# Optimization experiments

Hardware: AMD Instinct MI355X
Metric: run time of the kernel (lower is better)

Reference implementation:

```python
import jax, jax.numpy as jnp
import numpy as np

B, S, D, H = 1, 2048, 768, 12
E, K, I = 8, 2, 1024          # routed experts, top-k, expert inter dim
IS = 2 * I                    # shared-expert inter dim (n_shared_experts * moe_inter_dim)
EPS = 1e-5
ROUTE_SCALE = 1.0


def rmsnorm(x, w, eps=EPS):
    xf = x.astype(jnp.float32)
    return (xf * jax.lax.rsqrt(jnp.mean(xf * xf, axis=-1, keepdims=True) + eps)).astype(x.dtype) * w


def setup_inputs() -> dict:
    key = jax.random.key(0)
    ks = jax.random.split(key, 8)
    sc = 0.02
    return {
        "x": jax.random.normal(ks[0], (B, S, D), jnp.float32),
        "norm1_w": jnp.ones((D,), jnp.float32),
        "norm3_w": jnp.ones((D,), jnp.float32),
        "gate_w": jax.random.normal(ks[1], (E, D), jnp.float32) * sc,
        "w1": jax.random.normal(ks[2], (E, I, D), jnp.float32) * sc,
        "b1": jnp.zeros((E, I), jnp.float32),
        "w2": jax.random.normal(ks[3], (E, D, I), jnp.float32) * sc,
        "b2": jnp.zeros((E, D), jnp.float32),
        "w3": jax.random.normal(ks[4], (E, I, D), jnp.float32) * sc,
        "b3": jnp.zeros((E, I), jnp.float32),
        "fc1_w": jax.random.normal(ks[5], (IS, D), jnp.float32) * sc,
        "fc1_b": jnp.zeros((IS,), jnp.float32),
        "fc2_w": jax.random.normal(ks[6], (D, IS), jnp.float32) * sc,
        "fc2_b": jnp.zeros((D,), jnp.float32),
    }


def _forward(x, norm1_w, norm3_w, gate_w, w1, b1, w2, b2, w3, b3,
             fc1_w, fc1_b, fc2_w, fc2_b):
    b, s, d = x.shape
    hd = d // H

    # ---- self-attention (no qkv/out projections in the original module) ----
    xn = rmsnorm(x, norm1_w)
    qkv = xn.reshape(b, s, H, hd).transpose(0, 2, 1, 3)      # [b,h,s,hd]
    scores = jnp.einsum("bhqd,bhkd->bhqk", qkv, qkv) / np.sqrt(hd)
    attn = jax.nn.softmax(scores, axis=-1)
    ao = jnp.einsum("bhqk,bhkd->bhqd", attn, qkv)
    attn_out = ao.transpose(0, 2, 1, 3).reshape(b, s, d)
    out = x + attn_out

    # ---- MoE on norm3(out) ----
    xf = rmsnorm(out, norm3_w).reshape(-1, d)                # [N, D]
    n = xf.shape[0]

    # Gate: softmax scoring, n_groups=1 (no group masking), no bias (dim != 7168)
    logits = xf @ gate_w.T                                    # [N, E]
    sc = jax.nn.softmax(logits.astype(jnp.float32), axis=-1)  # max-subtract folded in
    _, idx = jax.lax.top_k(sc, K)                             # [N, K]
    weights = jnp.take_along_axis(sc, idx, axis=-1)
    weights = jnp.clip(weights, 1e-7) * ROUTE_SCALE
    weights = weights.astype(xf.dtype)

    # combine matrix: per-token dense expert weights (zeros for unselected)
    cmb = jnp.zeros((n, E), xf.dtype).at[jnp.arange(n)[:, None], idx].add(weights)

    # SwiGLU experts, batched over E (zero combine weight == not dispatched)
    a = jnp.einsum("nd,eid->nei", xf, w1) + b1                # [N,E,I]
    g = jnp.einsum("nd,eid->nei", xf, w3) + b3
    h = jax.nn.silu(a) * g
    eo = jnp.einsum("nei,edi->ned", h, w2) + b2               # [N,E,D]
    y = jnp.einsum("ned,ne->nd", eo, cmb)

    # shared experts (SiLU MLP)
    z = jax.nn.silu(xf @ fc1_w.T + fc1_b) @ fc2_w.T + fc2_b

    moe_out = (y + z).reshape(b, s, d)
    return out + moe_out


def reference(x, norm1_w, norm3_w, gate_w, w1, b1, w2, b2, w3, b3,
              fc1_w, fc1_b, fc2_w, fc2_b):
    return _forward(x, norm1_w, norm3_w, gate_w, w1, b1, w2, b2, w3, b3,
                    fc1_w, fc1_b, fc2_w, fc2_b)
```

## Files before the change

### kernel.cpp

```cpp
#include <hip/hip_runtime.h>
#include <math.h>

#define SEQ    2048
#define DMODEL 768
#define NHEAD  12
#define NEXP   8
#define IDIM   1024
#define ISH    2048
#define KVS    4
#define NE2    10

typedef unsigned short u16;
typedef short s16x8 __attribute__((ext_vector_type(8)));
typedef u16   u16x8 __attribute__((ext_vector_type(8)));
typedef float f32x4 __attribute__((ext_vector_type(4)));

#define MFMA_BF16(a, b, c) __builtin_amdgcn_mfma_f32_16x16x32_bf16((a), (b), (c), 0, 0, 0)

__device__ __forceinline__ void glds16(const void* g, void* l) {
  __builtin_amdgcn_global_load_lds(
      (const __attribute__((address_space(1))) unsigned int*)g,
      (__attribute__((address_space(3))) unsigned int*)l, 16, 0, 0);
}

__device__ __forceinline__ u16 f2b(float f) {
  unsigned int u = __float_as_uint(f);
  unsigned int r = u + 0x7fffu + ((u >> 16) & 1u);
  return (u16)(r >> 16);
}
__device__ __forceinline__ float b2f(u16 v) {
  return __uint_as_float(((unsigned int)v) << 16);
}

__global__ __launch_bounds__(256) void cvt_all_kernel(
    const float* __restrict__ w1, const float* __restrict__ w3, const float* __restrict__ w2,
    const float* __restrict__ fc1, const float* __restrict__ fc2,
    u16* __restrict__ w1b, u16* __restrict__ w3b, u16* __restrict__ w2b,
    u16* __restrict__ fc1b, u16* __restrict__ fc2b, int* __restrict__ counts) {
  if (blockIdx.x == 0 && threadIdx.x < 16) counts[threadIdx.x] = 0;
  long i = (long)blockIdx.x * 256 + threadIdx.x;
  const long NW8 = (long)NEXP * IDIM * DMODEL / 8;
  const long NF8 = (long)ISH * DMODEL / 8;
  const float* s; u16* d; long o;
  if      (i < NW8)             { s = w1;  d = w1b;  o = i; }
  else if (i < 2 * NW8)         { s = w3;  d = w3b;  o = i - NW8; }
  else if (i < 3 * NW8)         { s = w2;  d = w2b;  o = i - 2 * NW8; }
  else if (i < 3 * NW8 + NF8)   { s = fc1; d = fc1b; o = i - 3 * NW8; }
  else if (i < 3 * NW8 + 2*NF8) { s = fc2; d = fc2b; o = i - 3 * NW8 - NF8; }
  else return;
  float4 a = ((const float4*)s)[2 * o], b = ((const float4*)s)[2 * o + 1];
  u16x8 v;
  v[0] = f2b(a.x); v[1] = f2b(a.y); v[2] = f2b(a.z); v[3] = f2b(a.w);
  v[4] = f2b(b.x); v[5] = f2b(b.y); v[6] = f2b(b.z); v[7] = f2b(b.w);
  ((u16x8*)d)[o] = v;
}

__global__ __launch_bounds__(256) void rmsnorm_kernel(const float* __restrict__ in,
                                                      const float* __restrict__ w,
                                                      u16* __restrict__ outb) {
  int row = blockIdx.x;
  int tid = threadIdx.x;
  const float* r = in + (size_t)row * DMODEL;
  float v0 = r[tid], v1 = r[tid + 256], v2 = r[tid + 512];
  float ss = v0 * v0 + v1 * v1 + v2 * v2;
  __shared__ float red[256];
  red[tid] = ss;
  __syncthreads();
  for (int s = 128; s > 0; s >>= 1) {
    if (tid < s) red[tid] += red[tid + s];
    __syncthreads();
  }
  float rms = rsqrtf(red[0] * (1.f / DMODEL) + 1e-5f);
  u16* ob = outb + (size_t)row * DMODEL;
  ob[tid]       = f2b(v0 * rms * w[tid]);
  ob[tid + 256] = f2b(v1 * rms * w[tid + 256]);
  ob[tid + 512] = f2b(v2 * rms * w[tid + 512]);
}

__global__ __launch_bounds__(256) void attn_kernel(const u16* __restrict__ xnb,
                                                   u16* __restrict__ Opart,
                                                   float* __restrict__ Mpart,
                                                   float* __restrict__ Lpart) {
  __shared__ u16 Qs[64][72];
  __shared__ u16 Ks[64][72];
  __shared__ u16 Vt[64][72];
  __shared__ u16 Ps[64][72];
  const int h = blockIdx.y, kvs = blockIdx.z;
  const int q0 = blockIdx.x * 64;
  const int tid = threadIdx.x;
  const int lane = tid & 63, w = tid >> 6;
  const int quad = lane >> 4, l15 = lane & 15;
  const size_t hoff = (size_t)h * 64;

  for (int cc = tid; cc < 512; cc += 256) {
    int row = cc >> 3, col8 = (cc & 7) * 8;
    *(u16x8*)&Qs[row][col8] = *(const u16x8*)(xnb + (size_t)(q0 + row) * DMODEL + hoff + col8);
  }
  __syncthreads();
  const s16x8 aq0 = *(const s16x8*)&Qs[16 * w + l15][quad * 8];
  const s16x8 aq1 = *(const s16x8*)&Qs[16 * w + l15][32 + quad * 8];

  f32x4 o[4] = {};
  float mrow[4], lrow[4];
#pragma unroll
  for (int r = 0; r < 4; r++) { mrow[r] = -INFINITY; lrow[r] = 0.f; }

  const int it0 = kvs * (SEQ / 64 / KVS);
  for (int it = 0; it < SEQ / 64 / KVS; it++) {
    const int k0 = (it0 + it) * 64;
    for (int cc = tid; cc < 512; cc += 256) {
      int row = cc >> 3, col8 = (cc & 7) * 8;
      *(u16x8*)&Ks[row][col8] = *(const u16x8*)(xnb + (size_t)(k0 + row) * DMODEL + hoff + col8);
    }
    __syncthreads();

    {
      const int rp = tid & 31, dc = ((tid >> 5) & 7) * 8;
      u16x8 v0 = *(const u16x8*)&Ks[2 * rp][dc];
      u16x8 v1 = *(const u16x8*)&Ks[2 * rp + 1][dc];
#pragma unroll
      for (int j = 0; j < 8; j++) {
        *(unsigned int*)&Vt[dc + j][2 * rp] =
            (unsigned int)v0[j] | ((unsigned int)v1[j] << 16);
      }
    }

    f32x4 s4[4] = {};
#pragma unroll
    for (int jt = 0; jt < 4; jt++) {
      s16x8 b0 = *(const s16x8*)&Ks[16 * jt + l15][quad * 8];
      s16x8 b1 = *(const s16x8*)&Ks[16 * jt + l15][32 + quad * 8];
      s4[jt] = MFMA_BF16(aq0, b0, s4[jt]);
      s4[jt] = MFMA_BF16(aq1, b1, s4[jt]);
      s4[jt] *= 0.125f;
    }

#pragma unroll
    for (int r = 0; r < 4; r++) {
      float mx = mrow[r];
#pragma unroll
      for (int jt = 0; jt < 4; jt++) mx = fmaxf(mx, s4[jt][r]);
#pragma unroll
      for (int m = 1; m <= 8; m <<= 1) mx = fmaxf(mx, __shfl_xor(mx, m, 64));
      float al = __expf(mrow[r] - mx);
      mrow[r] = mx;
      float pv[4], sum = 0.f;
#pragma unroll
      for (int jt = 0; jt < 4; jt++) { pv[jt] = __expf(s4[jt][r] - mx); sum += pv[jt]; }
#pragma unroll
      for (int m = 1; m <= 8; m <<= 1) sum += __shfl_xor(sum, m, 64);
      lrow[r] = lrow[r] * al + sum;
#pragma unroll
      for (int jt = 0; jt < 4; jt++) o[jt][r] *= al;
#pragma unroll
      for (int jt = 0; jt < 4; jt++) Ps[16 * w + quad * 4 + r][16 * jt + l15] = f2b(pv[jt]);
    }
    __syncthreads();

    s16x8 ap0 = *(const s16x8*)&Ps[16 * w + l15][quad * 8];
    s16x8 ap1 = *(const s16x8*)&Ps[16 * w + l15][32 + quad * 8];
#pragma unroll
    for (int jt = 0; jt < 4; jt++) {
      s16x8 bv0 = *(const s16x8*)&Vt[16 * jt + l15][quad * 8];
      s16x8 bv1 = *(const s16x8*)&Vt[16 * jt + l15][32 + quad * 8];
      o[jt] = MFMA_BF16(ap0, bv0, o[jt]);
      o[jt] = MFMA_BF16(ap1, bv1, o[jt]);
    }
  }

  const size_t base = ((size_t)kvs * NHEAD + h) * SEQ;
#pragma unroll
  for (int r = 0; r < 4; r++) {
    int q = q0 + 16 * w + quad * 4 + r;
#pragma unroll
    for (int jt = 0; jt < 4; jt++)
      Opart[(base + q) * 64 + 16 * jt + l15] = f2b(o[jt][r]);
    if (l15 == 0) {
      Mpart[base + q] = mrow[r];
      Lpart[base + q] = lrow[r];
    }
  }
}

__global__ __launch_bounds__(256) void fused_post_kernel(
    const u16* __restrict__ Opart, const float* __restrict__ Mpart,
    const float* __restrict__ Lpart, const float* __restrict__ x,
    const float* __restrict__ n3w, const float* __restrict__ gw,
    u16* __restrict__ xfb, float* __restrict__ out,
    int* __restrict__ counts, int* __restrict__ toklist, float* __restrict__ wtlist) {
  const int t = blockIdx.x;
  const int tid = threadIdx.x;
  __shared__ float Ms[KVS * NHEAD], Ls[KVS * NHEAD];
  __shared__ float red[256];
  __shared__ float gred[4][NEXP];
  if (tid < KVS * NHEAD) {
    Ms[tid] = Mpart[(size_t)tid * SEQ + t];
    Ls[tid] = Lpart[(size_t)tid * SEQ + t];
  }
  __syncthreads();

  float val[3];
  float ss = 0.f;
#pragma unroll
  for (int ii = 0; ii < 3; ii++) {
    int c = tid + ii * 256;
    int h = c >> 6, d = c & 63;
    float M = -INFINITY;
#pragma unroll
    for (int k = 0; k < KVS; k++) M = fmaxf(M, Ms[k * NHEAD + h]);
    float L = 0.f, O = 0.f;
#pragma unroll
    for (int k = 0; k < KVS; k++) {
      float wgt = __expf(Ms[k * NHEAD + h] - M);
      L += wgt * Ls[k * NHEAD + h];
      O += wgt * b2f(Opart[((size_t)(k * NHEAD + h) * SEQ + t) * 64 + d]);
    }
    float v = x[(size_t)t * DMODEL + c] + O / L;
    out[(size_t)t * DMODEL + c] = v;
    val[ii] = v;
    ss += v * v;
  }
  red[tid] = ss;
  __syncthreads();
  for (int s = 128; s > 0; s >>= 1) {
    if (tid < s) red[tid] += red[tid + s];
    __syncthreads();
  }
  float rms = rsqrtf(red[0] * (1.f / DMODEL) + 1e-5f);

  float ge[NEXP] = {};
#pragma unroll
  for (int ii = 0; ii < 3; ii++) {
    int c = tid + ii * 256;
    float xn = val[ii] * rms * n3w[c];
    xfb[(size_t)t * DMODEL + c] = f2b(xn);
#pragma unroll
    for (int e = 0; e < NEXP; e++) ge[e] = fmaf(xn, gw[e * DMODEL + c], ge[e]);
  }
  const int lane = tid & 63, w = tid >> 6;
#pragma unroll
  for (int off = 32; off >= 1; off >>= 1)
#pragma unroll
    for (int e = 0; e < NEXP; e++) ge[e] += __shfl_xor(ge[e], off, 64);
  if (lane == 0)
#pragma unroll
    for (int e = 0; e < NEXP; e++) gred[w][e] = ge[e];
  __syncthreads();
  if (tid == 0) {
    float p[NEXP], mx = -INFINITY, s = 0.f;
#pragma unroll
    for (int e = 0; e < NEXP; e++) {
      p[e] = gred[0][e] + gred[1][e] + gred[2][e] + gred[3][e];
      mx = fmaxf(mx, p[e]);
    }
#pragma unroll
    for (int e = 0; e < NEXP; e++) { p[e] = __expf(p[e] - mx); s += p[e]; }
    int e0 = 0; float b0 = p[0];
    for (int e = 1; e < NEXP; e++) if (p[e] > b0) { b0 = p[e]; e0 = e; }
    int e1 = -1; float b1v = -1.f;
    for (int e = 0; e < NEXP; e++) if (e != e0 && p[e] > b1v) { b1v = p[e]; e1 = e; }
    float inv = 1.f / s;
    int pos0 = atomicAdd(&counts[e0], 1);
    toklist[e0 * SEQ + pos0] = t;
    wtlist[e0 * SEQ + pos0] = fmaxf(b0 * inv, 1e-7f);
    int pos1 = atomicAdd(&counts[e1], 1);
    toklist[e1 * SEQ + pos1] = t;
    wtlist[e1 * SEQ + pos1] = fmaxf(b1v * inv, 1e-7f);
  }
}

__global__ __launch_bounds__(256) void gemm1_kernel(
    const u16* __restrict__ xfb,
    const u16* __restrict__ w1b, const u16* __restrict__ w3b, const u16* __restrict__ fc1b,
    const float* __restrict__ b1, const float* __restrict__ b3, const float* __restrict__ fc1_b,
    const int* __restrict__ counts, const int* __restrict__ toklist, u16* __restrict__ hb) {
  __shared__ u16 As[64][32];
  __shared__ u16 W1s[128][32];
  __shared__ u16 W3s[128][32];
  __shared__ int rIdx[64];
  const int e = blockIdx.z;
  const bool routed = (e < NEXP);
  int cnt, off;
  if (routed) {
    cnt = counts[e];
    off = 0;
    for (int i = 0; i < e; i++) off += counts[i];
  } else {
    cnt = SEQ;
    off = 2 * SEQ + (e - NEXP) * SEQ;
  }
  const int m0 = blockIdx.y * 64;
  if (m0 >= cnt) return;
  const int n0 = blockIdx.x * 128;
  const int tid = threadIdx.x;
  if (tid < 64) {
    int rr = m0 + tid;
    rIdx[tid] = routed ? toklist[e * SEQ + (rr < cnt ? rr : cnt - 1)] : rr;
  }
  __syncthreads();
  const u16* W1 = routed ? w1b + (size_t)e * IDIM * DMODEL
                         : fc1b + (size_t)(e - NEXP) * IDIM * DMODEL;
  const u16* W3 = w3b + (size_t)(routed ? e : 0) * IDIM * DMODEL;

  const int lane = tid & 63, w = tid >> 6;
  const int quad = lane >> 4, l15 = lane & 15;
  const int wy = w >> 1, wx = w & 1;
  const int rsub = lane >> 2, c8 = (lane & 3) * 8;
  const u16* Ap   = xfb + (size_t)rIdx[16 * w + rsub] * DMODEL + c8;
  const u16* W1p0 = W1 + (size_t)(n0 + 32 * w + rsub) * DMODEL + c8;
  const u16* W1p1 = W1 + (size_t)(n0 + 32 * w + 16 + rsub) * DMODEL + c8;
  const u16* W3p0 = W3 + (size_t)(n0 + 32 * w + rsub) * DMODEL + c8;
  const u16* W3p1 = W3 + (size_t)(n0 + 32 * w + 16 + rsub) * DMODEL + c8;

  f32x4 acc1[2][4] = {};
  f32x4 acc3[2][4] = {};
  for (int k0 = 0; k0 < DMODEL; k0 += 32) {
    glds16(Ap + k0, &As[16 * w][0]);
    glds16(W1p0 + k0, &W1s[32 * w][0]);
    glds16(W1p1 + k0, &W1s[32 * w + 16][0]);
    if (routed) {
      glds16(W3p0 + k0, &W3s[32 * w][0]);
      glds16(W3p1 + k0, &W3s[32 * w + 16][0]);
    }
    __syncthreads();
    s16x8 af[2], w1f[4];
#pragma unroll
    for (int i = 0; i < 2; i++) af[i] = *(const s16x8*)&As[32 * wy + 16 * i + l15][quad * 8];
#pragma unroll
    for (int j = 0; j < 4; j++) w1f[j] = *(const s16x8*)&W1s[64 * wx + 16 * j + l15][quad * 8];
#pragma unroll
    for (int i = 0; i < 2; i++)
#pragma unroll
      for (int j = 0; j < 4; j++)
        acc1[i][j] = MFMA_BF16(af[i], w1f[j], acc1[i][j]);
    if (routed) {
      s16x8 w3f[4];
#pragma unroll
      for (int j = 0; j < 4; j++) w3f[j] = *(const s16x8*)&W3s[64 * wx + 16 * j + l15][quad * 8];
#pragma unroll
      for (int i = 0; i < 2; i++)
#pragma unroll
        for (int j = 0; j < 4; j++)
          acc3[i][j] = MFMA_BF16(af[i], w3f[j], acc3[i][j]);
    }
    __syncthreads();
  }

#pragma unroll
  for (int j = 0; j < 4; j++) {
    int n = n0 + 64 * wx + 16 * j + l15;
    float b1v = routed ? b1[e * IDIM + n] : fc1_b[(e - NEXP) * IDIM + n];
    float b3v = routed ? b3[e * IDIM + n] : 0.f;
#pragma unroll
    for (int i = 0; i < 2; i++) {
#pragma unroll
      for (int r = 0; r < 4; r++) {
        int rr = m0 + 32 * wy + 16 * i + quad * 4 + r;
        if (rr < cnt) {
          float a = acc1[i][j][r] + b1v;
          float g = routed ? (acc3[i][j][r] + b3v) : 1.f;
          float hv = a / (1.f + __expf(-a)) * g;
          hb[(size_t)(off + rr) * IDIM + n] = f2b(hv);
        }
      }
    }
  }
}

__global__ __launch_bounds__(256) void gemm2_kernel(
    const u16* __restrict__ hb,
    const u16* __restrict__ w2b, const u16* __restrict__ fc2b,
    const float* __restrict__ b2, const float* __restrict__ fc2_b,
    const int* __restrict__ counts, const int* __restrict__ toklist,
    const float* __restrict__ wtlist, float* __restrict__ out) {
  __shared__ u16 As[64][32];
  __shared__ u16 Ws[128][32];
  const int e = blockIdx.z;
  const bool routed = (e < NEXP);
  int cnt, off;
  if (routed) {
    cnt = counts[e];
    off = 0;
    for (int i = 0; i < e; i++) off += counts[i];
  } else {
    cnt = SEQ;
    off = 2 * SEQ + (e - NEXP) * SEQ;
  }
  const int m0 = blockIdx.y * 64;
  if (m0 >= cnt) return;
  const int n0 = blockIdx.x * 128;
  const int tid = threadIdx.x;

  const u16* Wb; int ldw, kof;
  if (routed) { Wb = w2b + (size_t)e * DMODEL * IDIM; ldw = IDIM; kof = 0; }
  else        { Wb = fc2b;                            ldw = ISH;  kof = (e - NEXP) * IDIM; }

  const int lane = tid & 63, w = tid >> 6;
  const int quad = lane >> 4, l15 = lane & 15;
  const int wy = w >> 1, wx = w & 1;
  const int rsub = lane >> 2, c8 = (lane & 3) * 8;
  int ra = m0 + 16 * w + rsub; ra = off + (ra < cnt ? ra : cnt - 1);
  const u16* Ap  = hb + (size_t)ra * IDIM + c8;
  const u16* Wp0 = Wb + (size_t)(n0 + 32 * w + rsub) * ldw + kof + c8;
  const u16* Wp1 = Wb + (size_t)(n0 + 32 * w + 16 + rsub) * ldw + kof + c8;

  f32x4 acc[2][4] = {};
  for (int k0 = 0; k0 < IDIM; k0 += 32) {
    glds16(Ap + k0, &As[16 * w][0]);
    glds16(Wp0 + k0, &Ws[32 * w][0]);
    glds16(Wp1 + k0, &Ws[32 * w + 16][0]);
    __syncthreads();
    s16x8 af[2], wf[4];
#pragma unroll
    for (int i = 0; i < 2; i++) af[i] = *(const s16x8*)&As[32 * wy + 16 * i + l15][quad * 8];
#pragma unroll
    for (int j = 0; j < 4; j++) wf[j] = *(const s16x8*)&Ws[64 * wx + 16 * j + l15][quad * 8];
#pragma unroll
    for (int i = 0; i < 2; i++)
#pragma unroll
      for (int j = 0; j < 4; j++)
        acc[i][j] = MFMA_BF16(af[i], wf[j], acc[i][j]);
    __syncthreads();
  }

#pragma unroll
  for (int j = 0; j < 4; j++) {
    int n = n0 + 64 * wx + 16 * j + l15;
    float bv = routed ? b2[e * DMODEL + n] : (e == NEXP ? fc2_b[n] : 0.f);
#pragma unroll
    for (int i = 0; i < 2; i++) {
#pragma unroll
      for (int r = 0; r < 4; r++) {
        int rr = m0 + 32 * wy + 16 * i + quad * 4 + r;
        if (rr < cnt) {
          int tok; float wt;
          if (routed) { tok = toklist[e * SEQ + rr]; wt = wtlist[e * SEQ + rr]; }
          else        { tok = rr;                    wt = 1.f; }
          atomicAdd(&out[(size_t)tok * DMODEL + n], wt * (acc[i][j][r] + bv));
        }
      }
    }
  }
}

extern "C" void kernel_launch(void* const* d_in, const int* in_sizes, int n_in,
                              void* d_out, int out_size, void* d_ws, size_t ws_size,
                              hipStream_t stream) {
  const float* x       = (const float*)d_in[0];
  const float* norm1_w = (const float*)d_in[1];
  const float* norm3_w = (const float*)d_in[2];
  const float* gate_w  = (const float*)d_in[3];
  const float* w1      = (const float*)d_in[4];
  const float* b1      = (const float*)d_in[5];
  const float* w2      = (const float*)d_in[6];
  const float* b2      = (const float*)d_in[7];
  const float* w3      = (const float*)d_in[8];
  const float* b3      = (const float*)d_in[9];
  const float* fc1_w   = (const float*)d_in[10];
  const float* fc1_b   = (const float*)d_in[11];
  const float* fc2_w   = (const float*)d_in[12];
  const float* fc2_b   = (const float*)d_in[13];
  float* out = (float*)d_out;

  char* p = (char*)d_ws;
  u16*   xnb    = (u16*)p;   p += (size_t)SEQ * DMODEL * 2;
  u16*   xfb    = (u16*)p;   p += (size_t)SEQ * DMODEL * 2;
  u16*   hb     = (u16*)p;   p += (size_t)4 * SEQ * IDIM * 2;
  u16*   Opart  = (u16*)p;   p += (size_t)KVS * NHEAD * SEQ * 64 * 2;
  float* Mpart  = (float*)p; p += (size_t)KVS * NHEAD * SEQ * 4;
  float* Lpart  = (float*)p; p += (size_t)KVS * NHEAD * SEQ * 4;
  u16*   w1b    = (u16*)p;   p += (size_t)NEXP * IDIM * DMODEL * 2;
  u16*   w3b    = (u16*)p;   p += (size_t)NEXP * IDIM * DMODEL * 2;
  u16*   w2b    = (u16*)p;   p += (size_t)NEXP * DMODEL * IDIM * 2;
  u16*   fc1b   = (u16*)p;   p += (size_t)ISH * DMODEL * 2;
  u16*   fc2b   = (u16*)p;   p += (size_t)DMODEL * ISH * 2;
  int*   counts = (int*)p;   p += 256;
  int*   toklist= (int*)p;   p += (size_t)NEXP * SEQ * 4;
  float* wtlist = (float*)p; p += (size_t)NEXP * SEQ * 4;

  const long NW8 = (long)NEXP * IDIM * DMODEL / 8;
  const long NF8 = (long)ISH * DMODEL / 8;
  const int cvt_blocks = (int)((3 * NW8 + 2 * NF8 + 255) / 256);
  cvt_all_kernel<<<cvt_blocks, 256, 0, stream>>>(w1, w3, w2, fc1_w, fc2_w,
                                                 w1b, w3b, w2b, fc1b, fc2b, counts);
  rmsnorm_kernel<<<SEQ, 256, 0, stream>>>(x, norm1_w, xnb);
  attn_kernel<<<dim3(SEQ / 64, NHEAD, KVS), 256, 0, stream>>>(xnb, Opart, Mpart, Lpart);
  fused_post_kernel<<<SEQ, 256, 0, stream>>>(Opart, Mpart, Lpart, x, norm3_w, gate_w,
                                             xfb, out, counts, toklist, wtlist);
  gemm1_kernel<<<dim3(IDIM / 128, SEQ / 64, NE2), 256, 0, stream>>>(
      xfb, w1b, w3b, fc1b, b1, b3, fc1_b, counts, toklist, hb);
  gemm2_kernel<<<dim3(DMODEL / 128, SEQ / 64, NE2), 256, 0, stream>>>(
      hb, w2b, fc2b, b2, fc2_b, counts, toklist, wtlist, out);
  (void)in_sizes; (void)n_in; (void)out_size; (void)ws_size;
}
```

Measured before the change: 352.6 us.

## Double-buffer MoE GEMMs with 64-wide swizzled LDS tiles and token-major attention partials

Both MoE GEMM kernels now stage K=64 tiles into two LDS buffers, prefetching the next tile while MFMAs consume the current one. An XOR swizzle on column chunks is meant to avoid LDS bank conflicts, and the grid is reordered so M blocks vary fastest. Attention partial outputs are stored token-major so the post kernel reads each token's partials contiguously. The cost is more LDS per block (W3 buffers are allocated even for shared-expert blocks), which may reduce occupancy.

New measurement: 521.9 us. 1.48x slower.

```diff
diff --git a/kernel.cpp b/kernel.cpp
--- a/kernel.cpp
+++ b/kernel.cpp
@@ -168,16 +168,17 @@
     }
   }
 
-  const size_t base = ((size_t)kvs * NHEAD + h) * SEQ;
+  const int hk = h * KVS + kvs;
 #pragma unroll
   for (int r = 0; r < 4; r++) {
     int q = q0 + 16 * w + quad * 4 + r;
+    size_t base = (size_t)q * (KVS * NHEAD) + hk;
 #pragma unroll
     for (int jt = 0; jt < 4; jt++)
-      Opart[(base + q) * 64 + 16 * jt + l15] = f2b(o[jt][r]);
+      Opart[base * 64 + 16 * jt + l15] = f2b(o[jt][r]);
     if (l15 == 0) {
-      Mpart[base + q] = mrow[r];
-      Lpart[base + q] = lrow[r];
+      Mpart[base] = mrow[r];
+      Lpart[base] = lrow[r];
     }
   }
 }
@@ -194,8 +195,8 @@
   __shared__ float red[256];
   __shared__ float gred[4][NEXP];
   if (tid < KVS * NHEAD) {
-    Ms[tid] = Mpart[(size_t)tid * SEQ + t];
-    Ls[tid] = Lpart[(size_t)tid * SEQ + t];
+    Ms[tid] = Mpart[(size_t)t * (KVS * NHEAD) + tid];
+    Ls[tid] = Lpart[(size_t)t * (KVS * NHEAD) + tid];
   }
   __syncthreads();
 
@@ -207,13 +208,13 @@
     int h = c >> 6, d = c & 63;
     float M = -INFINITY;
 #pragma unroll
-    for (int k = 0; k < KVS; k++) M = fmaxf(M, Ms[k * NHEAD + h]);
+    for (int k = 0; k < KVS; k++) M = fmaxf(M, Ms[h * KVS + k]);
     float L = 0.f, O = 0.f;
 #pragma unroll
     for (int k = 0; k < KVS; k++) {
-      float wgt = __expf(Ms[k * NHEAD + h] - M);
-      L += wgt * Ls[k * NHEAD + h];
-      O += wgt * b2f(Opart[((size_t)(k * NHEAD + h) * SEQ + t) * 64 + d]);
+      float wgt = __expf(Ms[h * KVS + k] - M);
+      L += wgt * Ls[h * KVS + k];
+      O += wgt * b2f(Opart[((size_t)t * (KVS * NHEAD) + h * KVS + k) * 64 + d]);
     }
     float v = x[(size_t)t * DMODEL + c] + O / L;
     out[(size_t)t * DMODEL + c] = v;
@@ -274,9 +275,9 @@
     const u16* __restrict__ w1b, const u16* __restrict__ w3b, const u16* __restrict__ fc1b,
     const float* __restrict__ b1, const float* __restrict__ b3, const float* __restrict__ fc1_b,
     const int* __restrict__ counts, const int* __restrict__ toklist, u16* __restrict__ hb) {
-  __shared__ u16 As[64][32];
-  __shared__ u16 W1s[128][32];
-  __shared__ u16 W3s[128][32];
+  __shared__ u16 As[2][64][64];
+  __shared__ u16 W1s[2][128][64];
+  __shared__ u16 W3s[2][128][64];
   __shared__ int rIdx[64];
   const int e = blockIdx.z;
   const bool routed = (e < NEXP);
@@ -289,9 +290,9 @@
     cnt = SEQ;
     off = 2 * SEQ + (e - NEXP) * SEQ;
   }
-  const int m0 = blockIdx.y * 64;
+  const int m0 = blockIdx.x * 64;
   if (m0 >= cnt) return;
-  const int n0 = blockIdx.x * 128;
+  const int n0 = blockIdx.y * 128;
   const int tid = threadIdx.x;
   if (tid < 64) {
     int rr = m0 + tid;
@@ -305,43 +306,66 @@
   const int lane = tid & 63, w = tid >> 6;
   const int quad = lane >> 4, l15 = lane & 15;
   const int wy = w >> 1, wx = w & 1;
-  const int rsub = lane >> 2, c8 = (lane & 3) * 8;
-  const u16* Ap   = xfb + (size_t)rIdx[16 * w + rsub] * DMODEL + c8;
-  const u16* W1p0 = W1 + (size_t)(n0 + 32 * w + rsub) * DMODEL + c8;
-  const u16* W1p1 = W1 + (size_t)(n0 + 32 * w + 16 + rsub) * DMODEL + c8;
-  const u16* W3p0 = W3 + (size_t)(n0 + 32 * w + rsub) * DMODEL + c8;
-  const u16* W3p1 = W3 + (size_t)(n0 + 32 * w + 16 + rsub) * DMODEL + c8;
+  const int lr = lane >> 3, ls = lane & 7;
+  const int swz8 = (ls ^ lr) << 3;
+  const int swzr = (l15 & 7) << 3;
+
+  const u16* aSrc[2];
+#pragma unroll
+  for (int c = 0; c < 2; c++) {
+    int tr = 16 * w + 8 * c + lr;
+    aSrc[c] = xfb + (size_t)rIdx[tr] * DMODEL + swz8;
+  }
+  const u16 *w1Src[4], *w3Src[4];
+#pragma unroll
+  for (int c = 0; c < 4; c++) {
+    int nr = n0 + 32 * w + 8 * c + lr;
+    w1Src[c] = W1 + (size_t)nr * DMODEL + swz8;
+    w3Src[c] = W3 + (size_t)nr * DMODEL + swz8;
+  }
+
+  auto stage = [&](int buf, int k0) {
+#pragma unroll
+    for (int c = 0; c < 2; c++) glds16(aSrc[c] + k0, &As[buf][16 * w + 8 * c][0]);
+#pragma unroll
+    for (int c = 0; c < 4; c++) glds16(w1Src[c] + k0, &W1s[buf][32 * w + 8 * c][0]);
+    if (routed) {
+#pragma unroll
+      for (int c = 0; c < 4; c++) glds16(w3Src[c] + k0, &W3s[buf][32 * w + 8 * c][0]);
+    }
+  };
 
   f32x4 acc1[2][4] = {};
   f32x4 acc3[2][4] = {};
-  for (int k0 = 0; k0 < DMODEL; k0 += 32) {
-    glds16(Ap + k0, &As[16 * w][0]);
-    glds16(W1p0 + k0, &W1s[32 * w][0]);
-    glds16(W1p1 + k0, &W1s[32 * w + 16][0]);
-    if (routed) {
-      glds16(W3p0 + k0, &W3s[32 * w][0]);
-      glds16(W3p1 + k0, &W3s[32 * w + 16][0]);
-    }
-    __syncthreads();
-    s16x8 af[2], w1f[4];
-#pragma unroll
-    for (int i = 0; i < 2; i++) af[i] = *(const s16x8*)&As[32 * wy + 16 * i + l15][quad * 8];
-#pragma unroll
-    for (int j = 0; j < 4; j++) w1f[j] = *(const s16x8*)&W1s[64 * wx + 16 * j + l15][quad * 8];
-#pragma unroll
-    for (int i = 0; i < 2; i++)
-#pragma unroll
-      for (int j = 0; j < 4; j++)
-        acc1[i][j] = MFMA_BF16(af[i], w1f[j], acc1[i][j]);
-    if (routed) {
-      s16x8 w3f[4];
-#pragma unroll
-      for (int j = 0; j < 4; j++) w3f[j] = *(const s16x8*)&W3s[64 * wx + 16 * j + l15][quad * 8];
+  stage(0, 0);
+  __syncthreads();
+  const int NK = DMODEL / 64;
+  for (int ks = 0; ks < NK; ks++) {
+    const int cur = ks & 1;
+    if (ks + 1 < NK) stage(cur ^ 1, (ks + 1) * 64);
+#pragma unroll
+    for (int kk = 0; kk < 2; kk++) {
+      const int cb = (kk * 32 + quad * 8) ^ swzr;
+      s16x8 af[2], w1f[4];
+#pragma unroll
+      for (int i = 0; i < 2; i++) af[i] = *(const s16x8*)&As[cur][32 * wy + 16 * i + l15][cb];
+#pragma unroll
+      for (int j = 0; j < 4; j++) w1f[j] = *(const s16x8*)&W1s[cur][64 * wx + 16 * j + l15][cb];
 #pragma unroll
       for (int i = 0; i < 2; i++)
 #pragma unroll
         for (int j = 0; j < 4; j++)
-          acc3[i][j] = MFMA_BF16(af[i], w3f[j], acc3[i][j]);
+          acc1[i][j] = MFMA_BF16(af[i], w1f[j], acc1[i][j]);
+      if (routed) {
+        s16x8 w3f[4];
+#pragma unroll
+        for (int j = 0; j < 4; j++) w3f[j] = *(const s16x8*)&W3s[cur][64 * wx + 16 * j + l15][cb];
+#pragma unroll
+        for (int i = 0; i < 2; i++)
+#pragma unroll
+          for (int j = 0; j < 4; j++)
+            acc3[i][j] = MFMA_BF16(af[i], w3f[j], acc3[i][j]);
+      }
     }
     __syncthreads();
   }
@@ -373,8 +397,8 @@
     const float* __restrict__ b2, const float* __restrict__ fc2_b,
     const int* __restrict__ counts, const int* __restrict__ toklist,
     const float* __restrict__ wtlist, float* __restrict__ out) {
-  __shared__ u16 As[64][32];
-  __shared__ u16 Ws[128][32];
+  __shared__ u16 As[2][64][64];
+  __shared__ u16 Ws[2][128][64];
   const int e = blockIdx.z;
   const bool routed = (e < NEXP);
   int cnt, off;
@@ -386,9 +410,9 @@
     cnt = SEQ;
     off = 2 * SEQ + (e - NEXP) * SEQ;
   }
-  const int m0 = blockIdx.y * 64;
+  const int m0 = blockIdx.x * 64;
   if (m0 >= cnt) return;
-  const int n0 = blockIdx.x * 128;
+  const int n0 = blockIdx.y * 128;
   const int tid = threadIdx.x;
 
   const u16* Wb; int ldw, kof;
@@ -398,28 +422,53 @@
   const int lane = tid & 63, w = tid >> 6;
   const int quad = lane >> 4, l15 = lane & 15;
   const int wy = w >> 1, wx = w & 1;
-  const int rsub = lane >> 2, c8 = (lane & 3) * 8;
-  int ra = m0 + 16 * w + rsub; ra = off + (ra < cnt ? ra : cnt - 1);
-  const u16* Ap  = hb + (size_t)ra * IDIM + c8;
-  const u16* Wp0 = Wb + (size_t)(n0 + 32 * w + rsub) * ldw + kof + c8;
-  const u16* Wp1 = Wb + (size_t)(n0 + 32 * w + 16 + rsub) * ldw + kof + c8;
+  const int lr = lane >> 3, ls = lane & 7;
+  const int swz8 = (ls ^ lr) << 3;
+  const int swzr = (l15 & 7) << 3;
+
+  const u16* aSrc[2];
+#pragma unroll
+  for (int c = 0; c < 2; c++) {
+    int tr = 16 * w + 8 * c + lr;
+    int ra = m0 + tr;
+    ra = off + (ra < cnt ? ra : cnt - 1);
+    aSrc[c] = hb + (size_t)ra * IDIM + swz8;
+  }
+  const u16* wSrc[4];
+#pragma unroll
+  for (int c = 0; c < 4; c++) {
+    int nr = n0 + 32 * w + 8 * c + lr;
+    wSrc[c] = Wb + (size_t)nr * ldw + kof + swz8;
+  }
+
+  auto stage = [&](int buf, int k0) {
+#pragma unroll
+    for (int c = 0; c < 2; c++) glds16(aSrc[c] + k0, &As[buf][16 * w + 8 * c][0]);
+#pragma unroll
+    for (int c = 0; c < 4; c++) glds16(wSrc[c] + k0, &Ws[buf][32 * w + 8 * c][0]);
+  };
 
   f32x4 acc[2][4] = {};
-  for (int k0 = 0; k0 < IDIM; k0 += 32) {
-    glds16(Ap + k0, &As[16 * w][0]);
-    glds16(Wp0 + k0, &Ws[32 * w][0]);
-    glds16(Wp1 + k0, &Ws[32 * w + 16][0]);
-    __syncthreads();
-    s16x8 af[2], wf[4];
-#pragma unroll
-    for (int i = 0; i < 2; i++) af[i] = *(const s16x8*)&As[32 * wy + 16 * i + l15][quad * 8];
-#pragma unroll
-    for (int j = 0; j < 4; j++) wf[j] = *(const s16x8*)&Ws[64 * wx + 16 * j + l15][quad * 8];
-#pragma unroll
-    for (int i = 0; i < 2; i++)
-#pragma unroll
-      for (int j = 0; j < 4; j++)
-        acc[i][j] = MFMA_BF16(af[i], wf[j], acc[i][j]);
+  stage(0, 0);
+  __syncthreads();
+  const int NK = IDIM / 64;
+  for (int ks = 0; ks < NK; ks++) {
+    const int cur = ks & 1;
+    if (ks + 1 < NK) stage(cur ^ 1, (ks + 1) * 64);
+#pragma unroll
+    for (int kk = 0; kk < 2; kk++) {
+      const int cb = (kk * 32 + quad * 8) ^ swzr;
+      s16x8 af[2], wf[4];
+#pragma unroll
+      for (int i = 0; i < 2; i++) af[i] = *(const s16x8*)&As[cur][32 * wy + 16 * i + l15][cb];
+#pragma unroll
+      for (int j = 0; j < 4; j++) wf[j] = *(const s16x8*)&Ws[cur][64 * wx + 16 * j + l15][cb];
+#pragma unroll
+      for (int i = 0; i < 2; i++)
+#pragma unroll
+        for (int j = 0; j < 4; j++)
+          acc[i][j] = MFMA_BF16(af[i], wf[j], acc[i][j]);
+    }
     __syncthreads();
   }
 
@@ -487,9 +536,9 @@
   attn_kernel<<<dim3(SEQ / 64, NHEAD, KVS), 256, 0, stream>>>(xnb, Opart, Mpart, Lpart);
   fused_post_kernel<<<SEQ, 256, 0, stream>>>(Opart, Mpart, Lpart, x, norm3_w, gate_w,
                                              xfb, out, counts, toklist, wtlist);
-  gemm1_kernel<<<dim3(IDIM / 128, SEQ / 64, NE2), 256, 0, stream>>>(
+  gemm1_kernel<<<dim3(SEQ / 64, IDIM / 128, NE2), 256, 0, stream>>>(
       xfb, w1b, w3b, fc1b, b1, b3, fc1_b, counts, toklist, hb);
-  gemm2_kernel<<<dim3(DMODEL / 128, SEQ / 64, NE2), 256, 0, stream>>>(
+  gemm2_kernel<<<dim3(SEQ / 64, DMODEL / 128, NE2), 256, 0, stream>>>(
       hb, w2b, fc2b, b2, fc2_b, counts, toklist, wtlist, out);
   (void)in_sizes; (void)n_in; (void)out_size; (void)ws_size;
 }
```
